# Performance work log

Hardware: AMD Instinct MI355X
Metric: run time of the kernel (lower is better)

Reference implementation:

```python
import jax, jax.numpy as jnp
import numpy as np

MIN_NORM = 1e-15
BALL_EPS_F32 = 0.004  # BALL_EPS[torch.float32]


def _norm(x):
    return jnp.maximum(jnp.linalg.norm(x, axis=-1, keepdims=True), MIN_NORM)


def project(x, c=1.0):
    norm = _norm(x)
    maxnorm = (1.0 - BALL_EPS_F32) / (c ** 0.5)
    return jnp.where(norm > maxnorm, x / norm * maxnorm, x)


def expmap0(u, c=1.0):
    sqrt_c = c ** 0.5
    un = _norm(u)
    gamma = jnp.tanh(jnp.clip(sqrt_c * un, -15.0, 15.0)) * u / (sqrt_c * un)
    return project(gamma, c)


def artanh(x):
    x = jnp.clip(x, -1.0 + 1e-5, 1.0 - 1e-5)
    return 0.5 * (jnp.log1p(x) - jnp.log1p(-x))


def logmap0(y, c=1.0):
    sqrt_c = c ** 0.5
    yn = _norm(y)
    return y / yn / sqrt_c * artanh(sqrt_c * yn)


def mobius_add(x, y, c=1.0):
    x2 = jnp.sum(x * x, axis=-1, keepdims=True)
    y2 = jnp.sum(y * y, axis=-1, keepdims=True)
    xy = jnp.sum(x * y, axis=-1, keepdims=True)
    num = (1 + 2 * c * xy + c * y2) * x + (1 - c * x2) * y
    denom = 1 + 2 * c * xy + (c ** 2) * x2 * y2
    return num / jnp.maximum(denom, MIN_NORM)


def p_exp_map(v):
    nv = jnp.maximum(jnp.linalg.norm(v, axis=-1, keepdims=True), 1e-10)
    return jnp.tanh(nv) * v / nv


def setup_inputs() -> dict:
    key = jax.random.key(0)
    ks = jax.random.split(key, 16)
    E, N, B = 1_000_000, 100_000, 512
    n_rel, D, A = 200, 64, 5
    R = 2 * n_rel + 1  # 401

    q_sub = jax.random.randint(ks[0], (B,), 0, N, dtype=jnp.int32)
    q_rel = jax.random.randint(ks[1], (B,), 0, R, dtype=jnp.int32)
    hidden = jax.random.normal(ks[2], (N, D), dtype=jnp.float32)

    r_idx = jax.random.randint(ks[3], (E,), 0, B, dtype=jnp.int32)
    rel = jax.random.randint(ks[4], (E,), 0, R, dtype=jnp.int32)
    sub = jax.random.randint(ks[5], (E,), 0, N, dtype=jnp.int32)
    obj = jax.random.randint(ks[6], (E,), 0, N, dtype=jnp.int32)
    dummy = jnp.zeros((E,), dtype=jnp.int32)
    edges = jnp.stack([r_idx, dummy, rel, dummy, sub, obj], axis=1)  # [E,6]

    s = 1.0 / np.sqrt(D)
    sa = 1.0 / np.sqrt(A)
    rela_embed = jax.random.normal(ks[7], (R, D), dtype=jnp.float32)
    query_embed = jax.random.normal(ks[8], (R, D), dtype=jnp.float32)
    Ws = jax.random.uniform(ks[9], (A, D), jnp.float32, -s, s)
    Wr = jax.random.uniform(ks[10], (A, D), jnp.float32, -s, s)
    Wqr_w = jax.random.uniform(ks[11], (A, D), jnp.float32, -s, s)
    Wqr_b = jax.random.uniform(ks[12], (A,), jnp.float32, -s, s)
    walpha_w = jax.random.uniform(ks[13], (1, A), jnp.float32, -sa, sa)
    walpha_b = jax.random.uniform(ks[14], (1,), jnp.float32, -sa, sa)
    Wh = jax.random.uniform(ks[15], (D, D), jnp.float32, -s, s)

    return {
        "q_sub": q_sub, "q_rel": q_rel, "hidden": hidden, "edges": edges,
        "n_node": N, "old_nodes_new_idx": jax.random.randint(jax.random.fold_in(key, 99), (100,), 0, N, dtype=jnp.int32),
        "rela_embed": rela_embed, "query_embed": query_embed,
        "Ws": Ws, "Wr": Wr, "Wqr_w": Wqr_w, "Wqr_b": Wqr_b,
        "walpha_w": walpha_w, "walpha_b": walpha_b, "Wh": Wh,
    }


def reference(q_sub, q_rel, hidden, edges, n_node, old_nodes_new_idx,
              rela_embed, query_embed, Ws, Wr, Wqr_w, Wqr_b,
              walpha_w, walpha_b, Wh):
    sub = edges[:, 4]
    rel = edges[:, 2]
    obj = edges[:, 5]
    r_idx = edges[:, 0]

    hs = hidden[sub]                     # [E, D] gather
    hr = rela_embed[rel]                 # [E, D]
    h_qr = query_embed[q_rel][r_idx]     # [E, D]

    # attention (note: bilinear/non_linear branch in the original is dead code)
    pre = hs @ Ws.T + hr @ Wr.T + (h_qr @ Wqr_w.T + Wqr_b)   # [E, A]
    alpha = jax.nn.sigmoid(jax.nn.relu(pre) @ walpha_w.T + walpha_b)  # [E, 1]

    hr_h = expmap0(hr, 1.0)
    hs_h = expmap0(hs, 1.0)
    message = logmap0(project(mobius_add(hs_h, hr_h, 1.0), 1.0), 1.0)
    message = alpha * message            # [E, D]

    message_agg = jax.ops.segment_sum(message, obj, num_segments=n_node)  # [N, D]
    a = message_agg @ Wh.T
    a = p_exp_map(a)
    hidden_new = logmap0(a, 1.0)         # act is identity
    return hidden_new
```

## Files before the change

kernel.cpp:

```cpp
#include <hip/hip_runtime.h>
#include <hip/hip_bf16.h>
#include <hip/hip_fp16.h>


__device__ __forceinline__ float wave_sum(float v) {
#pragma unroll
    for (int off = 32; off > 0; off >>= 1) v += __shfl_xor(v, off, 64);
    return v;
}

__device__ __forceinline__ float frcp(float x) {
#if __has_builtin(__builtin_amdgcn_rcpf)
    return __builtin_amdgcn_rcpf(x);
#else
    return 1.f / x;
#endif
}
__device__ __forceinline__ float fsqrt_(float x) {
#if __has_builtin(__builtin_amdgcn_sqrtf)
    return __builtin_amdgcn_sqrtf(x);
#else
    return sqrtf(x);
#endif
}
__device__ __forceinline__ float flog2_(float x) {
#if __has_builtin(__builtin_amdgcn_logf)
    return __builtin_amdgcn_logf(x);
#else
    return log2f(x);
#endif
}
__device__ __forceinline__ float fexp2_(float x) {
#if __has_builtin(__builtin_amdgcn_exp2f)
    return __builtin_amdgcn_exp2f(x);
#else
    return exp2f(x);
#endif
}

__device__ __forceinline__ unsigned pk2(float a, float b) {
    __half2 h = __floats2half2_rn(a, b);
    return __builtin_bit_cast(unsigned, h);
}
__device__ __forceinline__ float2 upk2(unsigned u) {
    __half2 h = __builtin_bit_cast(__half2, u);
    return __half22float2(h);
}

__device__ __forceinline__ void expmap0_scale(float norm, float& s, float& x2) {
    const float maxn = 1.0f - 0.004f;
    float un = fmaxf(norm, 1e-15f);
    float th = tanhf(fminf(un, 15.0f));
    float gs = th / un;
    float ng = gs * norm;
    float ps = ng > maxn ? maxn / ng : 1.0f;
    s = gs * ps;
    float sn = s * norm;
    x2 = sn * sn;
}


__global__ void prep_fused16(const int* __restrict__ q_rel,
                             const float* __restrict__ query_embed,
                             const float* __restrict__ Wqr_w,
                             const float* __restrict__ Wqr_b,
                             const float* __restrict__ rela_embed,
                             const float* __restrict__ Wr,
                             const float* __restrict__ hidden,
                             const float* __restrict__ Ws,
                             __half* __restrict__ hidden16,
                             uint4* __restrict__ hs_aux16,
                             __half* __restrict__ hr_h16,
                             uint4* __restrict__ hr_aux16,
                             uint4* __restrict__ preq16,
                             __half* __restrict__ agg16,
                             int N, int R, int B) {
    int wid = (blockIdx.x * blockDim.x + threadIdx.x) >> 6;
    int lane = threadIdx.x & 63;
    int nwaves = (N + 3) >> 2;
    if (wid < nwaves) {
        int q = lane >> 4, j = lane & 15;
        int n = wid * 4 + q;
        bool act = n < N;
        int nc = act ? n : N - 1;

        float4 u = *(const float4*)(hidden + (size_t)nc * 64 + 4 * j);
        float4 w0 = *(const float4*)(Ws + 0 * 64 + 4 * j);
        float4 w1 = *(const float4*)(Ws + 1 * 64 + 4 * j);
        float4 w2 = *(const float4*)(Ws + 2 * 64 + 4 * j);
        float4 w3 = *(const float4*)(Ws + 3 * 64 + 4 * j);
        float4 w4 = *(const float4*)(Ws + 4 * 64 + 4 * j);

#define DOT4(a, b) (fmaf((a).x, (b).x, fmaf((a).y, (b).y, fmaf((a).z, (b).z, (a).w * (b).w))))
        float p0 = DOT4(u, u);
        float p1 = DOT4(u, w0);
        float p2 = DOT4(u, w1);
        float p3 = DOT4(u, w2);
        float p4 = DOT4(u, w3);
        float p5 = DOT4(u, w4);
#undef DOT4
#pragma unroll
        for (int off = 1; off < 16; off <<= 1) {
            p0 += __shfl_xor(p0, off, 64);
            p1 += __shfl_xor(p1, off, 64);
            p2 += __shfl_xor(p2, off, 64);
            p3 += __shfl_xor(p3, off, 64);
            p4 += __shfl_xor(p4, off, 64);
            p5 += __shfl_xor(p5, off, 64);
        }
        float s, x2;
        expmap0_scale(fsqrt_(p0), s, x2);
        if (act) {
            uint2 hp; hp.x = pk2(u.x, u.y); hp.y = pk2(u.z, u.w);
            *(uint2*)(hidden16 + (size_t)n * 64 + 4 * j) = hp;
            uint2 zz; zz.x = 0u; zz.y = 0u;
            ((uint2*)(agg16 + (size_t)n * 64))[j] = zz;
            if (j == 0) {
                uint4 o; o.x = pk2(p1, p2); o.y = pk2(p3, p4); o.z = pk2(p5, 0.f); o.w = pk2(x2, s);
                hs_aux16[n] = o;
            }
        }
        return;
    }
    int w2 = wid - nwaves;
    if (w2 < R) {
        int r = w2;
        float u = rela_embed[r * 64 + lane];
        float p0 = u * u;
        float p1 = u * Wr[0 * 64 + lane];
        float p2 = u * Wr[1 * 64 + lane];
        float p3 = u * Wr[2 * 64 + lane];
        float p4 = u * Wr[3 * 64 + lane];
        float p5 = u * Wr[4 * 64 + lane];
#pragma unroll
        for (int off = 1; off < 64; off <<= 1) {
            p0 += __shfl_xor(p0, off, 64);
            p1 += __shfl_xor(p1, off, 64);
            p2 += __shfl_xor(p2, off, 64);
            p3 += __shfl_xor(p3, off, 64);
            p4 += __shfl_xor(p4, off, 64);
            p5 += __shfl_xor(p5, off, 64);
        }
        float s, y2;
        expmap0_scale(fsqrt_(p0), s, y2);
        hr_h16[r * 64 + lane] = __float2half(s * u);
        if (lane == 0) {
            uint4 o; o.x = pk2(p1, p2); o.y = pk2(p3, p4); o.z = pk2(p5, 0.f); o.w = pk2(y2, 0.f);
            hr_aux16[r] = o;
        }
    } else if (w2 < R + B) {
        int b = w2 - R;
        int qr = q_rel[b];
        float q = query_embed[qr * 64 + lane];
        float p1 = q * Wqr_w[0 * 64 + lane];
        float p2 = q * Wqr_w[1 * 64 + lane];
        float p3 = q * Wqr_w[2 * 64 + lane];
        float p4 = q * Wqr_w[3 * 64 + lane];
        float p5 = q * Wqr_w[4 * 64 + lane];
#pragma unroll
        for (int off = 1; off < 64; off <<= 1) {
            p1 += __shfl_xor(p1, off, 64);
            p2 += __shfl_xor(p2, off, 64);
            p3 += __shfl_xor(p3, off, 64);
            p4 += __shfl_xor(p4, off, 64);
            p5 += __shfl_xor(p5, off, 64);
        }
        if (lane == 0) {
            uint4 o;
            o.x = pk2(p1 + Wqr_b[0], p2 + Wqr_b[1]);
            o.y = pk2(p3 + Wqr_b[2], p4 + Wqr_b[3]);
            o.z = pk2(p5 + Wqr_b[4], 0.f);
            o.w = pk2(0.f, 0.f);
            preq16[b] = o;
        }
    }
}

__device__ __forceinline__ void edge_chain(
    unsigned hu_lo, unsigned hu_hi, unsigned yu_lo, unsigned yu_hi,
    uint4 hsa, uint4 hra, uint4 pqa,
    const float* wa, float wb,
    bool act, __half2* __restrict__ dst ) {
    float2 hs01 = upk2(hsa.x), hs23 = upk2(hsa.y), hs4 = upk2(hsa.z), hsxs = upk2(hsa.w);
    float2 hr01 = upk2(hra.x), hr23 = upk2(hra.y), hr4 = upk2(hra.z), hry = upk2(hra.w);
    float2 pq01 = upk2(pqa.x), pq23 = upk2(pqa.y), pq4 = upk2(pqa.z);
    float x2 = hsxs.x, s = hsxs.y, y2 = hry.x;

    float2 hl = upk2(hu_lo), hh = upk2(hu_hi);
    float2 yl = upk2(yu_lo), yh = upk2(yu_hi);

    float p = hl.x * yl.x;
    p = fmaf(hl.y, yl.y, p);
    p = fmaf(hh.x, yh.x, p);
    p = fmaf(hh.y, yh.y, p);
    p += __shfl_xor(p, 1, 64);
    p += __shfl_xor(p, 2, 64);
    p += __shfl_xor(p, 4, 64);
    p += __shfl_xor(p, 8, 64);
    float xy = p * s;

    float z = wb;
    z = fmaf(fmaxf(hs01.x + hr01.x + pq01.x, 0.f), wa[0], z);
    z = fmaf(fmaxf(hs01.y + hr01.y + pq01.y, 0.f), wa[1], z);
    z = fmaf(fmaxf(hs23.x + hr23.x + pq23.x, 0.f), wa[2], z);
    z = fmaf(fmaxf(hs23.y + hr23.y + pq23.y, 0.f), wa[3], z);
    z = fmaf(fmaxf(hs4.x + hr4.x + pq4.x, 0.f), wa[4], z);
    float alpha = frcp(1.f + fexp2_(z * -1.44269504f));

    float Af  = 1.f + 2.f * xy + y2;
    float Bf  = 1.f - x2;
    float den = fmaxf(1.f + 2.f * xy + x2 * y2, 1e-15f);
    float inv = frcp(den);
    float nm2 = fmaxf(fmaf(Af * Af, x2, fmaf(2.f * Af * Bf, xy, Bf * Bf * y2)), 0.f);
    float nm  = fsqrt_(nm2) * inv;
    const float maxn = 1.0f - 0.004f;
    float ps  = nm > maxn ? maxn * frcp(nm) : 1.f;
    float yn  = fmaxf(fminf(nm, maxn), 1e-15f);
    float ratio = (1.f + yn) * frcp(1.f - yn);
    float art = 0.34657359f * flog2_(ratio);
    float k  = inv * ps * alpha * art * frcp(yn);
    float cx = k * Af * s;
    float cy = k * Bf;

    __half2 q_lo = __floats2half2_rn(fmaf(cx, hl.x, cy * yl.x), fmaf(cx, hl.y, cy * yl.y));
    __half2 q_hi = __floats2half2_rn(fmaf(cx, hh.x, cy * yh.x), fmaf(cx, hh.y, cy * yh.y));
    if (act) {
        unsafeAtomicAdd(dst, q_lo);
        unsafeAtomicAdd(dst + 16, q_hi);
    }
}

__global__ __launch_bounds__(256) void edge_kernel8c(
    const int* __restrict__ edges,
    const __half* __restrict__ hidden16,
    const __half* __restrict__ hr_h16,
    const uint4* __restrict__ hs_aux16,
    const uint4* __restrict__ hr_aux16,
    const uint4* __restrict__ preq16,
    const float* __restrict__ walpha_w,
    const float* __restrict__ walpha_b,
    __half2* __restrict__ agg,
    int E)
{
    int wid = (blockIdx.x * blockDim.x + threadIdx.x) >> 6;
    int lane = threadIdx.x & 63;
    int g = lane >> 4;
    int j = lane & 15;

    int e0 = wid * 8 + g;
    int e1 = wid * 8 + 4 + g;
    bool act0 = e0 < E, act1 = e1 < E;
    int ec0 = act0 ? e0 : E - 1;
    int ec1 = act1 ? e1 : E - 1;

    const long long* er0 = (const long long*)(edges + (size_t)ec0 * 6);
    const long long* er1 = (const long long*)(edges + (size_t)ec1 * 6);
    long long a0 = __builtin_nontemporal_load(er0);
    long long b0 = __builtin_nontemporal_load(er0 + 1);
    long long c0 = __builtin_nontemporal_load(er0 + 2);
    long long a1 = __builtin_nontemporal_load(er1);
    long long b1 = __builtin_nontemporal_load(er1 + 1);
    long long c1 = __builtin_nontemporal_load(er1 + 2);
    int r0 = (int)a0, rel0 = (int)b0, sub0 = (int)c0, obj0 = (int)(c0 >> 32);
    int r1 = (int)a1, rel1 = (int)b1, sub1 = (int)c1, obj1 = (int)(c1 >> 32);

    uint4 hsa0 = hs_aux16[sub0];
    uint4 hra0 = hr_aux16[rel0];
    uint4 pqa0 = preq16[r0];
    uint4 hsa1 = hs_aux16[sub1];
    uint4 hra1 = hr_aux16[rel1];
    uint4 pqa1 = preq16[r1];

    const unsigned* hrow0 = (const unsigned*)(hidden16 + (size_t)sub0 * 64);
    const unsigned* yrow0 = (const unsigned*)(hr_h16 + (size_t)rel0 * 64);
    const unsigned* hrow1 = (const unsigned*)(hidden16 + (size_t)sub1 * 64);
    const unsigned* yrow1 = (const unsigned*)(hr_h16 + (size_t)rel1 * 64);
    unsigned hu_lo0 = hrow0[j], hu_hi0 = hrow0[16 + j];
    unsigned yu_lo0 = yrow0[j], yu_hi0 = yrow0[16 + j];
    unsigned hu_lo1 = hrow1[j], hu_hi1 = hrow1[16 + j];
    unsigned yu_lo1 = yrow1[j], yu_hi1 = yrow1[16 + j];

    float wa[5];
    wa[0] = walpha_w[0]; wa[1] = walpha_w[1]; wa[2] = walpha_w[2];
    wa[3] = walpha_w[3]; wa[4] = walpha_w[4];
    float wb = walpha_b[0];

    edge_chain(hu_lo0, hu_hi0, yu_lo0, yu_hi0, hsa0, hra0, pqa0, wa, wb,
               act0, agg + (size_t)obj0 * 32 + j);
    edge_chain(hu_lo1, hu_hi1, yu_lo1, yu_hi1, hsa1, hra1, pqa1, wa, wb,
               act1, agg + (size_t)obj1 * 32 + j);
}

__global__ __launch_bounds__(256) void final_gemm16(
    float* __restrict__ out,
    const __half* __restrict__ agg16,
    const float* __restrict__ Wh,
    int N)
{
    __shared__ __half tile[64 * 64];
    int t = threadIdx.x;
    int lane = t & 63;
    int w = t >> 6;

    float wh[64];
    const float4* whr = (const float4*)(Wh + (size_t)lane * 64);
#pragma unroll
    for (int i = 0; i < 16; ++i) {
        float4 v = whr[i];
        wh[4 * i] = v.x; wh[4 * i + 1] = v.y; wh[4 * i + 2] = v.z; wh[4 * i + 3] = v.w;
    }

    int ntiles = (N + 63) >> 6;
    for (int ti = blockIdx.x; ti < ntiles; ti += gridDim.x) {
        int base = ti << 6;
        int nrow = min(64, N - base);
        __syncthreads();
        {
            const uint2* src = (const uint2*)(agg16 + (size_t)base * 64);
            uint2* dst = (uint2*)tile;
            int nu2 = nrow * 16;
            for (int i = t; i < nu2; i += 256) dst[i] = src[i];
        }
        __syncthreads();
#pragma unroll 1
        for (int r = 0; r < 16; ++r) {
            int n = base + w * 16 + r;
            if (n >= N) break;
            const uint2* arow = (const uint2*)(tile + (w * 16 + r) * 64);
            float acc = 0.f;
#pragma unroll
            for (int kk = 0; kk < 16; ++kk) {
                uint2 u = arow[kk];
                float2 f0 = upk2(u.x), f1 = upk2(u.y);
                acc = fmaf(f0.x, wh[4 * kk], acc);
                acc = fmaf(f0.y, wh[4 * kk + 1], acc);
                acc = fmaf(f1.x, wh[4 * kk + 2], acc);
                acc = fmaf(f1.y, wh[4 * kk + 3], acc);
            }
            float n2 = wave_sum(acc * acc);
            float na = fsqrt_(n2);
            float nv = fmaxf(na, 1e-10f);
            float pn = tanhf(nv);
            float rinv = frcp(nv);
            float pp = pn * acc * rinv;
            float np = pn * (na * rinv);
            float yn = fmaxf(np, 1e-15f);
            float tt = fminf(yn, 1.f - 1e-5f);
            float ratio = (1.f + tt) * frcp(1.f - tt);
            float art = 0.34657359f * flog2_(ratio);
            out[(size_t)n * 64 + lane] = pp * art * frcp(yn);
        }
    }
}


__global__ void prep_small_kernel(const int* __restrict__ q_rel,
                                  const float* __restrict__ query_embed,
                                  const float* __restrict__ Wqr_w,
                                  const float* __restrict__ Wqr_b,
                                  const float* __restrict__ rela_embed,
                                  const float* __restrict__ Wr,
                                  float* __restrict__ hr_h,
                                  float* __restrict__ hr_aux,
                                  float* __restrict__ preq,
                                  int R, int B, int A) {
    int w = (blockIdx.x * blockDim.x + threadIdx.x) >> 6;
    int lane = threadIdx.x & 63;
    if (w < R) {
        int r = w;
        float u = rela_embed[r * 64 + lane];
        float n2 = wave_sum(u * u);
        float s, y2;
        expmap0_scale(fsqrt_(n2), s, y2);
        hr_h[r * 64 + lane] = s * u;
        for (int a = 0; a < A; ++a) {
            float p = wave_sum(u * Wr[a * 64 + lane]);
            if (lane == 0) hr_aux[r * 8 + a] = p;
        }
        if (lane == 0) hr_aux[r * 8 + 6] = y2;
    } else if (w < R + B) {
        int b = w - R;
        int qr = q_rel[b];
        float q = query_embed[qr * 64 + lane];
        for (int a = 0; a < A; ++a) {
            float p = wave_sum(q * Wqr_w[a * 64 + lane]);
            if (lane == 0) preq[b * 8 + a] = p + Wqr_b[a];
        }
    }
}

__global__ void prep_node_kernel(const float* __restrict__ hidden,
                                 const float* __restrict__ Ws,
                                 float* __restrict__ hs_aux, int N, int A) {
    int w = (blockIdx.x * blockDim.x + threadIdx.x) >> 6;
    if (w >= N) return;
    int lane = threadIdx.x & 63;
    float u = hidden[(size_t)w * 64 + lane];
    float n2 = wave_sum(u * u);
    float s, x2;
    expmap0_scale(fsqrt_(n2), s, x2);
    for (int a = 0; a < A; ++a) {
        float p = wave_sum(u * Ws[a * 64 + lane]);
        if (lane == 0) hs_aux[w * 8 + a] = p;
    }
    if (lane == 0) { hs_aux[w * 8 + 6] = x2; hs_aux[w * 8 + 7] = s; }
}

__global__ void edge_kernel_f32(const int* __restrict__ edges,
                                const float* __restrict__ hidden,
                                const float* __restrict__ hr_h,
                                const float* __restrict__ hr_aux,
                                const float* __restrict__ hs_aux,
                                const float* __restrict__ preq,
                                const float* __restrict__ walpha_w,
                                const float* __restrict__ walpha_b,
                                float* __restrict__ agg,
                                int E, int A) {
    int w = (blockIdx.x * blockDim.x + threadIdx.x) >> 6;
    if (w >= E) return;
    int lane = threadIdx.x & 63;
    const int* er = edges + (size_t)w * 6;
    int r_idx = er[0], rel = er[2], sub = er[4], obj = er[5];

    float s  = hs_aux[(size_t)sub * 8 + 7];
    float x2 = hs_aux[(size_t)sub * 8 + 6];
    float h  = hidden[(size_t)sub * 64 + lane];
    float x  = h * s;
    float y  = hr_h[(size_t)rel * 64 + lane];
    float y2 = hr_aux[(size_t)rel * 8 + 6];
    float xy = wave_sum(x * y);

    float z = walpha_b[0];
    for (int a = 0; a < A; ++a) {
        float pre = hs_aux[(size_t)sub * 8 + a] + hr_aux[(size_t)rel * 8 + a] + preq[(size_t)r_idx * 8 + a];
        z += fmaxf(pre, 0.f) * walpha_w[a];
    }
    float alpha = frcp(1.f + fexp2_(z * -1.44269504f));

    float Af = 1.f + 2.f * xy + y2;
    float Bf = 1.f - x2;
    float den = fmaxf(1.f + 2.f * xy + x2 * y2, 1e-15f);
    float inv = frcp(den);
    float nm2 = fmaxf(Af * Af * x2 + 2.f * Af * Bf * xy + Bf * Bf * y2, 0.f);
    float nm = fsqrt_(nm2) * inv;
    const float maxn = 1.0f - 0.004f;
    float ps = nm > maxn ? maxn * frcp(nm) : 1.f;
    float yn = fmaxf(fminf(nm, maxn), 1e-15f);
    float ratio = (1.f + yn) * frcp(1.f - yn);
    float art = 0.34657359f * flog2_(ratio);
    float k = inv * ps * alpha * art * frcp(yn);
    float msg = fmaf(k * Af * s, h, k * Bf * y);
    unsafeAtomicAdd(agg + (size_t)obj * 64 + lane, msg);
}

__global__ void final_kernel_f32(float* __restrict__ out,
                                 const float* __restrict__ Wh,
                                 int N) {
    __shared__ float WhT[64 * 64];
    int t = threadIdx.x;
    for (int i = t; i < 64 * 64; i += blockDim.x) {
        int row = i >> 6, col = i & 63;
        WhT[col * 64 + row] = Wh[i];
    }
    __syncthreads();

    int lane = t & 63;
    int wl = t >> 6;
    int wpb = blockDim.x >> 6;
    int wg = blockIdx.x * wpb + wl;
    int wstride = gridDim.x * wpb;

    for (int n = wg; n < N; n += wstride) {
        float v = out[(size_t)n * 64 + lane];
        float a = 0.f;
#pragma unroll
        for (int k = 0; k < 64; ++k)
            a = fmaf(__shfl(v, k, 64), WhT[k * 64 + lane], a);

        float n2 = wave_sum(a * a);
        float na = fsqrt_(n2);
        float nv = fmaxf(na, 1e-10f);
        float pn = tanhf(nv);
        float rinv = frcp(nv);
        float pp = pn * a * rinv;
        float np = pn * (na * rinv);
        float yn = fmaxf(np, 1e-15f);
        float tt = fminf(yn, 1.f - 1e-5f);
        float ratio = (1.f + tt) * frcp(1.f - tt);
        float art = 0.34657359f * flog2_(ratio);
        out[(size_t)n * 64 + lane] = pp * art * frcp(yn);
    }
}

extern "C" void kernel_launch(void* const* d_in, const int* in_sizes, int n_in,
                              void* d_out, int out_size, void* d_ws, size_t ws_size,
                              hipStream_t stream) {
    const int*   q_rel       = (const int*)d_in[1];
    const float* hidden      = (const float*)d_in[2];
    const int*   edges       = (const int*)d_in[3];
    const float* rela_embed  = (const float*)d_in[6];
    const float* query_embed = (const float*)d_in[7];
    const float* Ws          = (const float*)d_in[8];
    const float* Wr          = (const float*)d_in[9];
    const float* Wqr_w       = (const float*)d_in[10];
    const float* Wqr_b       = (const float*)d_in[11];
    const float* walpha_w    = (const float*)d_in[12];
    const float* walpha_b    = (const float*)d_in[13];
    const float* Wh          = (const float*)d_in[14];

    const int D = 64;
    int B = in_sizes[0];
    int E = in_sizes[3] / 6;
    int A = in_sizes[11];
    int R = in_sizes[6] / D;
    int N = out_size / D;

    float* out = (float*)d_out;

    size_t agg_b    = (size_t)N * 64 * 2;
    size_t hid16_b  = (size_t)N * 64 * 2;
    size_t hsaux_b  = (size_t)N * 16;
    size_t hrh_b    = (size_t)R * 64 * 2;
    size_t hraux_b  = (size_t)R * 16;
    size_t preq_b   = (size_t)B * 16;
    size_t need16   = agg_b + hid16_b + hsaux_b + hrh_b + hraux_b + preq_b;
    bool f16path = (A == 5) && (ws_size >= need16);

    if (f16path) {
        char* base = (char*)d_ws;
        __half2* agg      = (__half2*)base;                 base += agg_b;
        __half*  hidden16 = (__half*)base;                  base += hid16_b;
        uint4*   hs_aux16 = (uint4*)base;                   base += hsaux_b;
        __half*  hr_h16   = (__half*)base;                  base += hrh_b;
        uint4*   hr_aux16 = (uint4*)base;                   base += hraux_b;
        uint4*   preq16   = (uint4*)base;

        int nwaves = (N + 3) / 4;
        int total_waves = nwaves + R + B;
        prep_fused16<<<(total_waves + 3) / 4, 256, 0, stream>>>(
            q_rel, query_embed, Wqr_w, Wqr_b, rela_embed, Wr,
            hidden, Ws, hidden16, hs_aux16, hr_h16, hr_aux16, preq16,
            (__half*)agg, N, R, B);

        int ewaves = (E + 7) / 8;
        edge_kernel8c<<<(ewaves + 3) / 4, 256, 0, stream>>>(
            edges, hidden16, hr_h16, hs_aux16, hr_aux16, preq16,
            walpha_w, walpha_b, agg, E);

        final_gemm16<<<1024, 256, 0, stream>>>(out, (const __half*)agg, Wh, N);
    } else {
        float* hs_aux = (float*)d_ws;
        float* hr_h   = hs_aux + (size_t)N * 8;
        float* hr_aux = hr_h + (size_t)R * 64;
        float* preq   = hr_aux + (size_t)R * 8;

        hipMemsetAsync(d_out, 0, (size_t)out_size * sizeof(float), stream);

        int waves_small = R + B;
        prep_small_kernel<<<(waves_small * 64 + 255) / 256, 256, 0, stream>>>(
            q_rel, query_embed, Wqr_w, Wqr_b, rela_embed, Wr,
            hr_h, hr_aux, preq, R, B, A);

        prep_node_kernel<<<(N + 3) / 4, 256, 0, stream>>>(hidden, Ws, hs_aux, N, A);

        edge_kernel_f32<<<(E + 3) / 4, 256, 0, stream>>>(
            edges, hidden, hr_h, hr_aux, hs_aux, preq,
            walpha_w, walpha_b, out, E, A);

        final_kernel_f32<<<1024, 256, 0, stream>>>(out, Wh, N);
    }
}
```

Baseline: 161.7 us.

## Bucket edges by destination node block and aggregate messages in LDS

Adds a counting-sort style pass that packs each edge into 64 bits and scatters it into per-128-node buckets of fixed capacity, with an overflow buffer. A per-bucket kernel then computes messages and accumulates them with fp32 LDS atomics before writing fp16 aggregates once, and a small kernel handles overflow edges with global atomics. This is meant to replace a million scattered fp16 global atomics with local ones and to drop the agg zeroing, at the cost of an extra scatter pass, an extra kernel launch and bucket-buffer traffic. The packed-index limits gate the path, and it falls back to the old path when they fail.

Measured after the change: 537.5 us. +232.5%, slower.

```diff
diff --git a/kernel.cpp b/kernel.cpp
--- a/kernel.cpp
+++ b/kernel.cpp
@@ -57,6 +57,80 @@
     s = gs * ps;
     float sn = s * norm;
     x2 = sn * sn;
+}
+
+__device__ __forceinline__ float2 edge_coef(
+    unsigned hu_lo, unsigned hu_hi, unsigned yu_lo, unsigned yu_hi,
+    uint4 hsa, uint4 hra, uint4 pqa, const float* wa, float wb) {
+    float2 hs01 = upk2(hsa.x), hs23 = upk2(hsa.y), hs4 = upk2(hsa.z), hsxs = upk2(hsa.w);
+    float2 hr01 = upk2(hra.x), hr23 = upk2(hra.y), hr4 = upk2(hra.z), hry = upk2(hra.w);
+    float2 pq01 = upk2(pqa.x), pq23 = upk2(pqa.y), pq4 = upk2(pqa.z);
+    float x2 = hsxs.x, s = hsxs.y, y2 = hry.x;
+
+    float2 hl = upk2(hu_lo), hh = upk2(hu_hi);
+    float2 yl = upk2(yu_lo), yh = upk2(yu_hi);
+
+    float p = hl.x * yl.x;
+    p = fmaf(hl.y, yl.y, p);
+    p = fmaf(hh.x, yh.x, p);
+    p = fmaf(hh.y, yh.y, p);
+    p += __shfl_xor(p, 1, 64);
+    p += __shfl_xor(p, 2, 64);
+    p += __shfl_xor(p, 4, 64);
+    p += __shfl_xor(p, 8, 64);
+    float xy = p * s;
+
+    float z = wb;
+    z = fmaf(fmaxf(hs01.x + hr01.x + pq01.x, 0.f), wa[0], z);
+    z = fmaf(fmaxf(hs01.y + hr01.y + pq01.y, 0.f), wa[1], z);
+    z = fmaf(fmaxf(hs23.x + hr23.x + pq23.x, 0.f), wa[2], z);
+    z = fmaf(fmaxf(hs23.y + hr23.y + pq23.y, 0.f), wa[3], z);
+    z = fmaf(fmaxf(hs4.x + hr4.x + pq4.x, 0.f), wa[4], z);
+    float alpha = frcp(1.f + fexp2_(z * -1.44269504f));
+
+    float Af  = 1.f + 2.f * xy + y2;
+    float Bf  = 1.f - x2;
+    float den = fmaxf(1.f + 2.f * xy + x2 * y2, 1e-15f);
+    float inv = frcp(den);
+    float nm2 = fmaxf(fmaf(Af * Af, x2, fmaf(2.f * Af * Bf, xy, Bf * Bf * y2)), 0.f);
+    float nm  = fsqrt_(nm2) * inv;
+    const float maxn = 1.0f - 0.004f;
+    float ps  = nm > maxn ? maxn * frcp(nm) : 1.f;
+    float yn  = fmaxf(fminf(nm, maxn), 1e-15f);
+    float ratio = (1.f + yn) * frcp(1.f - yn);
+    float art = 0.34657359f * flog2_(ratio);
+    float k  = inv * ps * alpha * art * frcp(yn);
+    return make_float2(k * Af * s, k * Bf);
+}
+
+__device__ __forceinline__ void edge_to_lds(
+    unsigned hu_lo, unsigned hu_hi, unsigned yu_lo, unsigned yu_hi,
+    uint4 hsa, uint4 hra, uint4 pqa, const float* wa, float wb,
+    bool act, float* aggrow , int j) {
+    float2 c = edge_coef(hu_lo, hu_hi, yu_lo, yu_hi, hsa, hra, pqa, wa, wb);
+    float2 hl = upk2(hu_lo), hh = upk2(hu_hi);
+    float2 yl = upk2(yu_lo), yh = upk2(yu_hi);
+    if (act) {
+        atomicAdd(&aggrow[2 * j],      fmaf(c.x, hl.x, c.y * yl.x));
+        atomicAdd(&aggrow[2 * j + 1],  fmaf(c.x, hl.y, c.y * yl.y));
+        atomicAdd(&aggrow[32 + 2 * j], fmaf(c.x, hh.x, c.y * yh.x));
+        atomicAdd(&aggrow[33 + 2 * j], fmaf(c.x, hh.y, c.y * yh.y));
+    }
+}
+
+__device__ __forceinline__ void edge_to_global(
+    unsigned hu_lo, unsigned hu_hi, unsigned yu_lo, unsigned yu_hi,
+    uint4 hsa, uint4 hra, uint4 pqa, const float* wa, float wb,
+    bool act, __half2* dst ) {
+    float2 c = edge_coef(hu_lo, hu_hi, yu_lo, yu_hi, hsa, hra, pqa, wa, wb);
+    float2 hl = upk2(hu_lo), hh = upk2(hu_hi);
+    float2 yl = upk2(yu_lo), yh = upk2(yu_hi);
+    __half2 q_lo = __floats2half2_rn(fmaf(c.x, hl.x, c.y * yl.x), fmaf(c.x, hl.y, c.y * yl.y));
+    __half2 q_hi = __floats2half2_rn(fmaf(c.x, hh.x, c.y * yh.x), fmaf(c.x, hh.y, c.y * yh.y));
+    if (act) {
+        unsafeAtomicAdd(dst, q_lo);
+        unsafeAtomicAdd(dst + 16, q_hi);
+    }
 }
 
 
@@ -74,7 +148,7 @@
                              uint4* __restrict__ hr_aux16,
                              uint4* __restrict__ preq16,
                              __half* __restrict__ agg16,
-                             int N, int R, int B) {
+                             int N, int R, int B, int zero_agg) {
     int wid = (blockIdx.x * blockDim.x + threadIdx.x) >> 6;
     int lane = threadIdx.x & 63;
     int nwaves = (N + 3) >> 2;
@@ -113,8 +187,10 @@
         if (act) {
             uint2 hp; hp.x = pk2(u.x, u.y); hp.y = pk2(u.z, u.w);
             *(uint2*)(hidden16 + (size_t)n * 64 + 4 * j) = hp;
-            uint2 zz; zz.x = 0u; zz.y = 0u;
-            ((uint2*)(agg16 + (size_t)n * 64))[j] = zz;
+            if (zero_agg) {
+                uint2 zz; zz.x = 0u; zz.y = 0u;
+                ((uint2*)(agg16 + (size_t)n * 64))[j] = zz;
+            }
             if (j == 0) {
                 uint4 o; o.x = pk2(p1, p2); o.y = pk2(p3, p4); o.z = pk2(p5, 0.f); o.w = pk2(x2, s);
                 hs_aux16[n] = o;
@@ -176,57 +252,160 @@
     }
 }
 
-__device__ __forceinline__ void edge_chain(
-    unsigned hu_lo, unsigned hu_hi, unsigned yu_lo, unsigned yu_hi,
-    uint4 hsa, uint4 hra, uint4 pqa,
-    const float* wa, float wb,
-    bool act, __half2* __restrict__ dst ) {
-    float2 hs01 = upk2(hsa.x), hs23 = upk2(hsa.y), hs4 = upk2(hsa.z), hsxs = upk2(hsa.w);
-    float2 hr01 = upk2(hra.x), hr23 = upk2(hra.y), hr4 = upk2(hra.z), hry = upk2(hra.w);
-    float2 pq01 = upk2(pqa.x), pq23 = upk2(pqa.y), pq4 = upk2(pqa.z);
-    float x2 = hsxs.x, s = hsxs.y, y2 = hry.x;
-
-    float2 hl = upk2(hu_lo), hh = upk2(hu_hi);
-    float2 yl = upk2(yu_lo), yh = upk2(yu_hi);
-
-    float p = hl.x * yl.x;
-    p = fmaf(hl.y, yl.y, p);
-    p = fmaf(hh.x, yh.x, p);
-    p = fmaf(hh.y, yh.y, p);
-    p += __shfl_xor(p, 1, 64);
-    p += __shfl_xor(p, 2, 64);
-    p += __shfl_xor(p, 4, 64);
-    p += __shfl_xor(p, 8, 64);
-    float xy = p * s;
-
-    float z = wb;
-    z = fmaf(fmaxf(hs01.x + hr01.x + pq01.x, 0.f), wa[0], z);
-    z = fmaf(fmaxf(hs01.y + hr01.y + pq01.y, 0.f), wa[1], z);
-    z = fmaf(fmaxf(hs23.x + hr23.x + pq23.x, 0.f), wa[2], z);
-    z = fmaf(fmaxf(hs23.y + hr23.y + pq23.y, 0.f), wa[3], z);
-    z = fmaf(fmaxf(hs4.x + hr4.x + pq4.x, 0.f), wa[4], z);
-    float alpha = frcp(1.f + fexp2_(z * -1.44269504f));
-
-    float Af  = 1.f + 2.f * xy + y2;
-    float Bf  = 1.f - x2;
-    float den = fmaxf(1.f + 2.f * xy + x2 * y2, 1e-15f);
-    float inv = frcp(den);
-    float nm2 = fmaxf(fmaf(Af * Af, x2, fmaf(2.f * Af * Bf, xy, Bf * Bf * y2)), 0.f);
-    float nm  = fsqrt_(nm2) * inv;
-    const float maxn = 1.0f - 0.004f;
-    float ps  = nm > maxn ? maxn * frcp(nm) : 1.f;
-    float yn  = fmaxf(fminf(nm, maxn), 1e-15f);
-    float ratio = (1.f + yn) * frcp(1.f - yn);
-    float art = 0.34657359f * flog2_(ratio);
-    float k  = inv * ps * alpha * art * frcp(yn);
-    float cx = k * Af * s;
-    float cy = k * Bf;
-
-    __half2 q_lo = __floats2half2_rn(fmaf(cx, hl.x, cy * yl.x), fmaf(cx, hl.y, cy * yl.y));
-    __half2 q_hi = __floats2half2_rn(fmaf(cx, hh.x, cy * yh.x), fmaf(cx, hh.y, cy * yh.y));
-    if (act) {
-        unsafeAtomicAdd(dst, q_lo);
-        unsafeAtomicAdd(dst + 16, q_hi);
+
+__global__ void init_cur(int* __restrict__ cur, int NB, int cap) {
+    int i = blockIdx.x * blockDim.x + threadIdx.x;
+    if (i < NB) cur[i] = i * cap;
+    else if (i == NB) cur[i] = 0;
+}
+
+__global__ __launch_bounds__(256) void scatter_edges(
+    const int* __restrict__ edges, int E, int NB, int cap,
+    int* __restrict__ cur,
+    unsigned long long* __restrict__ bbuf,
+    unsigned long long* __restrict__ ovfbuf, int ovfcap)
+{
+    __shared__ unsigned long long spk[4096];
+    __shared__ int lh[1024];
+    __shared__ int lb[1024];
+    int t = threadIdx.x;
+    int base = blockIdx.x * 4096;
+    for (int i = t; i < NB; i += 256) lh[i] = 0;
+    __syncthreads();
+    int nloc = min(4096, E - base);
+    for (int k = t; k < nloc; k += 256) {
+        const long long* er = (const long long*)(edges + (size_t)(base + k) * 6);
+        long long a = er[0], bq = er[1], cq = er[2];
+        int ri = (int)a, rel = (int)bq, sub = (int)cq, obj = (int)(cq >> 32);
+        unsigned long long pk = (unsigned long long)(unsigned)(obj & 0x1ffff)
+            | ((unsigned long long)(unsigned)(sub & 0x1ffff) << 17)
+            | ((unsigned long long)(unsigned)(rel & 0x1ff) << 34)
+            | ((unsigned long long)(unsigned)(ri & 0x1ff) << 43);
+        spk[k] = pk;
+        atomicAdd(&lh[obj >> 7], 1);
+    }
+    __syncthreads();
+    for (int i = t; i < NB; i += 256) {
+        int c = lh[i];
+        lb[i] = c ? atomicAdd(&cur[i], c) : 0;
+    }
+    __syncthreads();
+    for (int i = t; i < NB; i += 256) lh[i] = 0;
+    __syncthreads();
+    for (int k = t; k < nloc; k += 256) {
+        unsigned long long pk = spk[k];
+        int bk = (int)(pk & 0x1ffff) >> 7;
+        int rank = atomicAdd(&lh[bk], 1);
+        int slot = lb[bk] + rank;
+        if (slot < (bk + 1) * cap) {
+            bbuf[slot] = pk;
+        } else {
+            int o = atomicAdd(cur + NB, 1);
+            if (o < ovfcap) ovfbuf[o] = pk;
+        }
+    }
+}
+
+__global__ __launch_bounds__(256) void bucket_edge(
+    const unsigned long long* __restrict__ bbuf,
+    const int* __restrict__ cur, int cap, int N,
+    const __half* __restrict__ hidden16,
+    const __half* __restrict__ hr_h16,
+    const uint4* __restrict__ hs_aux16,
+    const uint4* __restrict__ hr_aux16,
+    const uint4* __restrict__ preq16,
+    const float* __restrict__ walpha_w,
+    const float* __restrict__ walpha_b,
+    __half* __restrict__ agg16)
+{
+    __shared__ float agg[128 * 65];
+    int b = blockIdx.x;
+    int t = threadIdx.x;
+    for (int i = t; i < 128 * 65; i += 256) agg[i] = 0.f;
+
+    float wa[5];
+    wa[0] = walpha_w[0]; wa[1] = walpha_w[1]; wa[2] = walpha_w[2];
+    wa[3] = walpha_w[3]; wa[4] = walpha_w[4];
+    float wb = walpha_b[0];
+
+    __syncthreads();
+
+    int start = b * cap;
+    int cnt = min(cur[b] - start, cap);
+    int lane = t & 63;
+    int w = t >> 6;
+    int g = lane >> 4;
+    int j = lane & 15;
+
+    for (int it = w * 8; it < cnt; it += 32) {
+        int i0 = it + g, i1 = it + 4 + g;
+        bool a0 = i0 < cnt, a1 = i1 < cnt;
+        unsigned long long p0 = bbuf[start + (a0 ? i0 : 0)];
+        unsigned long long p1 = bbuf[start + (a1 ? i1 : 0)];
+        int obj0 = (int)(p0 & 0x1ffff), sub0 = (int)((p0 >> 17) & 0x1ffff);
+        int rel0 = (int)((p0 >> 34) & 0x1ff), ri0 = (int)((p0 >> 43) & 0x1ff);
+        int obj1 = (int)(p1 & 0x1ffff), sub1 = (int)((p1 >> 17) & 0x1ffff);
+        int rel1 = (int)((p1 >> 34) & 0x1ff), ri1 = (int)((p1 >> 43) & 0x1ff);
+
+        uint4 hsa0 = hs_aux16[sub0], hra0 = hr_aux16[rel0], pqa0 = preq16[ri0];
+        uint4 hsa1 = hs_aux16[sub1], hra1 = hr_aux16[rel1], pqa1 = preq16[ri1];
+        const unsigned* hrow0 = (const unsigned*)(hidden16 + (size_t)sub0 * 64);
+        const unsigned* yrow0 = (const unsigned*)(hr_h16 + (size_t)rel0 * 64);
+        const unsigned* hrow1 = (const unsigned*)(hidden16 + (size_t)sub1 * 64);
+        const unsigned* yrow1 = (const unsigned*)(hr_h16 + (size_t)rel1 * 64);
+        unsigned hu_lo0 = hrow0[j], hu_hi0 = hrow0[16 + j];
+        unsigned yu_lo0 = yrow0[j], yu_hi0 = yrow0[16 + j];
+        unsigned hu_lo1 = hrow1[j], hu_hi1 = hrow1[16 + j];
+        unsigned yu_lo1 = yrow1[j], yu_hi1 = yrow1[16 + j];
+
+        edge_to_lds(hu_lo0, hu_hi0, yu_lo0, yu_hi0, hsa0, hra0, pqa0, wa, wb,
+                    a0, agg + (obj0 & 127) * 65, j);
+        edge_to_lds(hu_lo1, hu_hi1, yu_lo1, yu_hi1, hsa1, hra1, pqa1, wa, wb,
+                    a1, agg + (obj1 & 127) * 65, j);
+    }
+    __syncthreads();
+
+    int nbase = b << 7;
+    for (int i = t; i < 128 * 32; i += 256) {
+        int r = i >> 5, c = i & 31;
+        int n = nbase + r;
+        if (n < N) {
+            unsigned v = pk2(agg[r * 65 + 2 * c], agg[r * 65 + 2 * c + 1]);
+            ((unsigned*)(agg16 + (size_t)n * 64))[c] = v;
+        }
+    }
+}
+
+__global__ __launch_bounds__(256) void ovf_edge(
+    const unsigned long long* __restrict__ ovfbuf,
+    const int* __restrict__ ovfcnt_p, int ovfcap,
+    const __half* __restrict__ hidden16,
+    const __half* __restrict__ hr_h16,
+    const uint4* __restrict__ hs_aux16,
+    const uint4* __restrict__ hr_aux16,
+    const uint4* __restrict__ preq16,
+    const float* __restrict__ walpha_w,
+    const float* __restrict__ walpha_b,
+    __half2* __restrict__ agg)
+{
+    int cnt = min(*ovfcnt_p, ovfcap);
+    if (cnt <= 0) return;
+    int j = threadIdx.x & 15;
+    int qid = (blockIdx.x * blockDim.x + threadIdx.x) >> 4;
+    int nq = (gridDim.x * blockDim.x) >> 4;
+    float wa[5];
+    wa[0] = walpha_w[0]; wa[1] = walpha_w[1]; wa[2] = walpha_w[2];
+    wa[3] = walpha_w[3]; wa[4] = walpha_w[4];
+    float wb = walpha_b[0];
+    for (int e = qid; e < cnt; e += nq) {
+        unsigned long long pk = ovfbuf[e];
+        int obj = (int)(pk & 0x1ffff), sub = (int)((pk >> 17) & 0x1ffff);
+        int rel = (int)((pk >> 34) & 0x1ff), ri = (int)((pk >> 43) & 0x1ff);
+        uint4 hsa = hs_aux16[sub], hra = hr_aux16[rel], pqa = preq16[ri];
+        const unsigned* hrow = (const unsigned*)(hidden16 + (size_t)sub * 64);
+        const unsigned* yrow = (const unsigned*)(hr_h16 + (size_t)rel * 64);
+        edge_to_global(hrow[j], hrow[16 + j], yrow[j], yrow[16 + j],
+                       hsa, hra, pqa, wa, wb, true, agg + (size_t)obj * 32 + j);
     }
 }
 
@@ -264,31 +443,23 @@
     int r0 = (int)a0, rel0 = (int)b0, sub0 = (int)c0, obj0 = (int)(c0 >> 32);
     int r1 = (int)a1, rel1 = (int)b1, sub1 = (int)c1, obj1 = (int)(c1 >> 32);
 
-    uint4 hsa0 = hs_aux16[sub0];
-    uint4 hra0 = hr_aux16[rel0];
-    uint4 pqa0 = preq16[r0];
-    uint4 hsa1 = hs_aux16[sub1];
-    uint4 hra1 = hr_aux16[rel1];
-    uint4 pqa1 = preq16[r1];
+    uint4 hsa0 = hs_aux16[sub0], hra0 = hr_aux16[rel0], pqa0 = preq16[r0];
+    uint4 hsa1 = hs_aux16[sub1], hra1 = hr_aux16[rel1], pqa1 = preq16[r1];
 
     const unsigned* hrow0 = (const unsigned*)(hidden16 + (size_t)sub0 * 64);
     const unsigned* yrow0 = (const unsigned*)(hr_h16 + (size_t)rel0 * 64);
     const unsigned* hrow1 = (const unsigned*)(hidden16 + (size_t)sub1 * 64);
     const unsigned* yrow1 = (const unsigned*)(hr_h16 + (size_t)rel1 * 64);
-    unsigned hu_lo0 = hrow0[j], hu_hi0 = hrow0[16 + j];
-    unsigned yu_lo0 = yrow0[j], yu_hi0 = yrow0[16 + j];
-    unsigned hu_lo1 = hrow1[j], hu_hi1 = hrow1[16 + j];
-    unsigned yu_lo1 = yrow1[j], yu_hi1 = yrow1[16 + j];
 
     float wa[5];
     wa[0] = walpha_w[0]; wa[1] = walpha_w[1]; wa[2] = walpha_w[2];
     wa[3] = walpha_w[3]; wa[4] = walpha_w[4];
     float wb = walpha_b[0];
 
-    edge_chain(hu_lo0, hu_hi0, yu_lo0, yu_hi0, hsa0, hra0, pqa0, wa, wb,
-               act0, agg + (size_t)obj0 * 32 + j);
-    edge_chain(hu_lo1, hu_hi1, yu_lo1, yu_hi1, hsa1, hra1, pqa1, wa, wb,
-               act1, agg + (size_t)obj1 * 32 + j);
+    edge_to_global(hrow0[j], hrow0[16 + j], yrow0[j], yrow0[16 + j],
+                   hsa0, hra0, pqa0, wa, wb, act0, agg + (size_t)obj0 * 32 + j);
+    edge_to_global(hrow1[j], hrow1[16 + j], yrow1[j], yrow1[16 + j],
+                   hsa1, hra1, pqa1, wa, wb, act1, agg + (size_t)obj1 * 32 + j);
 }
 
 __global__ __launch_bounds__(256) void final_gemm16(
@@ -517,30 +688,74 @@
 
     float* out = (float*)d_out;
 
-    size_t agg_b    = (size_t)N * 64 * 2;
-    size_t hid16_b  = (size_t)N * 64 * 2;
+    size_t agg_b    = (size_t)N * 128;
+    size_t hid16_b  = (size_t)N * 128;
     size_t hsaux_b  = (size_t)N * 16;
-    size_t hrh_b    = (size_t)R * 64 * 2;
+    size_t hrh_b    = (size_t)R * 128;
     size_t hraux_b  = (size_t)R * 16;
     size_t preq_b   = (size_t)B * 16;
     size_t need16   = agg_b + hid16_b + hsaux_b + hrh_b + hraux_b + preq_b;
-    bool f16path = (A == 5) && (ws_size >= need16);
-
-    if (f16path) {
+
+    int NB = (N + 127) >> 7;
+    int cap = 2 * ((E + NB - 1) / (NB > 0 ? NB : 1));
+    if (cap < 512) cap = 512;
+    int ovfcap = 65536;
+    size_t bbuf_b = (size_t)NB * (size_t)cap * 8;
+    size_t cur_b  = (((size_t)NB + 1) * 4 + 15) & ~(size_t)15;
+    size_t ovf_b  = (size_t)ovfcap * 8;
+    size_t need_bucket = need16 + bbuf_b + cur_b + ovf_b;
+
+    bool pack_ok = (N > 0) && (N <= 131072) && (R <= 512) && (B <= 512) &&
+                   (NB <= 1024) && (E > 0) && ((long long)NB * cap < (1LL << 31));
+
+    if (A == 5 && pack_ok && ws_size >= need_bucket) {
         char* base = (char*)d_ws;
-        __half2* agg      = (__half2*)base;                 base += agg_b;
-        __half*  hidden16 = (__half*)base;                  base += hid16_b;
-        uint4*   hs_aux16 = (uint4*)base;                   base += hsaux_b;
-        __half*  hr_h16   = (__half*)base;                  base += hrh_b;
-        uint4*   hr_aux16 = (uint4*)base;                   base += hraux_b;
-        uint4*   preq16   = (uint4*)base;
+        __half* agg16    = (__half*)base;            base += agg_b;
+        __half* hidden16 = (__half*)base;            base += hid16_b;
+        uint4*  hs_aux16 = (uint4*)base;             base += hsaux_b;
+        __half* hr_h16   = (__half*)base;            base += hrh_b;
+        uint4*  hr_aux16 = (uint4*)base;             base += hraux_b;
+        uint4*  preq16   = (uint4*)base;             base += preq_b;
+        unsigned long long* bbuf = (unsigned long long*)base; base += bbuf_b;
+        int* cur = (int*)base;                       base += cur_b;
+        unsigned long long* ovfbuf = (unsigned long long*)base;
+
+        init_cur<<<(NB + 1 + 255) / 256, 256, 0, stream>>>(cur, NB, cap);
 
         int nwaves = (N + 3) / 4;
         int total_waves = nwaves + R + B;
         prep_fused16<<<(total_waves + 3) / 4, 256, 0, stream>>>(
             q_rel, query_embed, Wqr_w, Wqr_b, rela_embed, Wr,
             hidden, Ws, hidden16, hs_aux16, hr_h16, hr_aux16, preq16,
-            (__half*)agg, N, R, B);
+            agg16, N, R, B, 0);
+
+        scatter_edges<<<(E + 4095) / 4096, 256, 0, stream>>>(
+            edges, E, NB, cap, cur, bbuf, ovfbuf, ovfcap);
+
+        bucket_edge<<<NB, 256, 0, stream>>>(
+            bbuf, cur, cap, N, hidden16, hr_h16, hs_aux16, hr_aux16, preq16,
+            walpha_w, walpha_b, agg16);
+
+        ovf_edge<<<64, 256, 0, stream>>>(
+            ovfbuf, cur + NB, ovfcap, hidden16, hr_h16, hs_aux16, hr_aux16,
+            preq16, walpha_w, walpha_b, (__half2*)agg16);
+
+        final_gemm16<<<1024, 256, 0, stream>>>(out, agg16, Wh, N);
+    } else if (A == 5 && ws_size >= need16) {
+        char* base = (char*)d_ws;
+        __half2* agg      = (__half2*)base;          base += agg_b;
+        __half*  hidden16 = (__half*)base;           base += hid16_b;
+        uint4*   hs_aux16 = (uint4*)base;            base += hsaux_b;
+        __half*  hr_h16   = (__half*)base;           base += hrh_b;
+        uint4*   hr_aux16 = (uint4*)base;            base += hraux_b;
+        uint4*   preq16   = (uint4*)base;
+
+        int nwaves = (N + 3) / 4;
+        int total_waves = nwaves + R + B;
+        prep_fused16<<<(total_waves + 3) / 4, 256, 0, stream>>>(
+            q_rel, query_embed, Wqr_w, Wqr_b, rela_embed, Wr,
+            hidden, Ws, hidden16, hs_aux16, hr_h16, hr_aux16, preq16,
+            (__half*)agg, N, R, B, 1);
 
         int ewaves = (E + 7) / 8;
         edge_kernel8c<<<(ewaves + 3) / 4, 256, 0, stream>>>(
```
